# Performance work log

Hardware: AMD Instinct MI355X
Metric: run time of the kernel (lower is better)

Reference implementation:

```python
import jax, jax.numpy as jnp
import numpy as np

N_IMG = 512
N_ANGLES = 180


def _bilinear(img, sy, sx):
    """Bilinear sample img at float coords (sy, sx); zero outside the image."""
    n = img.shape[0]
    y0 = jnp.floor(sy)
    x0 = jnp.floor(sx)
    wy = sy - y0
    wx = sx - x0
    y0i = y0.astype(jnp.int32)
    x0i = x0.astype(jnp.int32)

    def gather(yi, xi):
        valid = (yi >= 0) & (yi < n) & (xi >= 0) & (xi < n)
        yc = jnp.clip(yi, 0, n - 1)
        xc = jnp.clip(xi, 0, n - 1)
        return jnp.where(valid, img[yc, xc], jnp.zeros((), img.dtype))

    v00 = gather(y0i, x0i)
    v01 = gather(y0i, x0i + 1)
    v10 = gather(y0i + 1, x0i)
    v11 = gather(y0i + 1, x0i + 1)
    return (v00 * (1 - wy) * (1 - wx) + v01 * (1 - wy) * wx
            + v10 * wy * (1 - wx) + v11 * wy * wx)


def _radon(img, angles):
    """skimage-style radon: rotate image by each angle, sum along axis 0.
    Returns sinogram of shape (n_detectors, n_angles) = (N, len(angles))."""
    n = img.shape[0]
    c = (n - 1) * 0.5  # rotation about image center
    coords = jnp.arange(n, dtype=img.dtype) - c
    yc, xc = jnp.meshgrid(coords, coords, indexing="ij")  # (N, N)

    def one_angle(theta_deg):
        t = jnp.deg2rad(theta_deg.astype(img.dtype))
        co, si = jnp.cos(t), jnp.sin(t)
        # inverse-rotation sampling coordinates (CCW rotation of the image)
        sx = co * xc + si * yc + c
        sy = -si * xc + co * yc + c
        rotated = _bilinear(img, sy, sx)  # (N, N)
        return rotated.sum(axis=0)        # projection along detector rows -> (N,)

    sino = jax.vmap(one_angle)(angles)  # (n_angles, N)
    return sino.T                        # (N, n_angles)


def setup_inputs() -> dict:
    key = jax.random.key(0)
    img = jax.random.uniform(key, (N_IMG, N_IMG), dtype=jnp.float32)  # nonnegative PET activity
    angles = jnp.arange(N_ANGLES, dtype=jnp.int32)  # degrees 0..179 (skimage default)
    return {"img": img, "angles": angles}


def reference(img, angles):
    return _radon(img, angles)
```

## Files before the change

kernel.cpp:

```cpp
#include <hip/hip_runtime.h>
#include <hip/hip_fp16.h>
#include <stdint.h>

#define N 512
#define NA 180
#define TD 64
#define TI 512
#define TW 96
#define TILE_DW (36 * 256)
#define PP 708
#define PR 704
#define POFF 96

#define WS_IMGPB  0
#define WS_IMGTPB (PR * PP)
#define WS_TAB    (2 * PR * PP)
#define WS_FLAGS  (WS_TAB + 4 * NA)

typedef _Float16 hh2 __attribute__((ext_vector_type(2)));
union H2U { uint32_t u; hh2 h; };

__device__ __forceinline__ hh2 cvt_pkrtz(float a, float b) {
    return __builtin_bit_cast(hh2, __builtin_amdgcn_cvt_pkrtz(a, b));
}

__device__ __forceinline__ void load16_to_lds(const uint32_t* g, uint32_t* l) {
    __builtin_amdgcn_global_load_lds(
        (const __attribute__((address_space(1))) void*)g,
        (__attribute__((address_space(3))) void*)l,
        16 , 0 , 0 );
}

__global__ __launch_bounds__(512) void pad_kernel(const float* __restrict__ img,
                                                  const int* __restrict__ angles,
                                                  uint32_t* __restrict__ imgPB,
                                                  uint32_t* __restrict__ imgTPB,
                                                  float4* __restrict__ tab,
                                                  int* __restrict__ flags) {
    __shared__ float lds[65 * 66];
    const int tid  = threadIdx.x;
    const int lane = tid & 63;
    const int wq   = tid >> 6;
    const int bx = blockIdx.x, by = blockIdx.y;
    const int b  = by * 11 + bx;

    if (b == 120 && tid < NA) {
        float t = (float)angles[tid] * 0.017453292519943295f;
        float si = sinf(t), co = cosf(t);
        int useT = fabsf(si) > fabsf(co);
        float4 e;
        if (useT) { e.x = co; e.y = -si; e.z = si; e.w = co; }
        else      { e.x = si; e.y = co;  e.z = co; e.w = -si; }
        tab[tid] = e;
        flags[tid] = useT;
    }

    for (int idx = tid; idx < 65 * 65; idx += 512) {
        int r = idx / 65, cc = idx - r * 65;
        int y = by * 64 + r - POFF, x = bx * 64 + cc - POFF;
        bool in = ((unsigned)y < N) && ((unsigned)x < N);
        lds[r * 66 + cc] = in ? img[y * N + x] : 0.0f;
    }
    __syncthreads();
#pragma unroll
    for (int j = 0; j < 8; ++j) {
        int r = wq * 8 + j;
        float v0 = lds[r * 66 + lane], v1 = lds[r * 66 + lane + 1];
        __half2 h = __halves2half2(__float2half(v0), __float2half(v1));
        imgPB[(size_t)(by * 64 + r) * PP + bx * 64 + lane] = *(uint32_t*)&h;
        float t0 = lds[lane * 66 + r], t1 = lds[(lane + 1) * 66 + r];
        __half2 ht = __halves2half2(__float2half(t0), __float2half(t1));
        imgTPB[(size_t)(bx * 64 + r) * PP + by * 64 + lane] = *(uint32_t*)&ht;
    }
}

__global__ __launch_bounds__(512, 8) void radon_kernel(const uint32_t* __restrict__ imgPB,
                                                       const uint32_t* __restrict__ imgTPB,
                                                       const float4* __restrict__ tab,
                                                       const int* __restrict__ flags,
                                                       float* __restrict__ out) {
    __shared__ uint32_t tile[TILE_DW];

    const int tid  = threadIdx.x;
    const int lane = tid & 63;
    const int wave = tid >> 6;
    const int d0 = blockIdx.x * TD;
    const int a  = blockIdx.y;
    const int rot = (blockIdx.x + blockIdx.y) & 7;

    const float c = 255.5f;
    const float4 tb = tab[a];
    const float au = tb.x, bus = tb.y, av = tb.z, bvs = tb.w;

    const float xc0 = (float)d0 - c, xc1 = (float)(d0 + TD - 1) - c;
    const float buA = fmaf(bus, xc0, c), buB = fmaf(bus, xc1, c);
    const float bvA = fmaf(bvs, xc0, c), bvB = fmaf(bvs, xc1, c);
    const float buMin = fminf(buA, buB), buMax = fmaxf(buA, buB);
    const float bvMin = fminf(bvA, bvB), bvMax = fmaxf(bvA, bvB);

    const uint32_t* __restrict__ src = flags[a] ? imgTPB : imgPB;

    const float xcl = (float)(d0 + lane) - c;
    const float buLb = fmaf(bus, xcl, c);
    const float bvLb = fmaf(bvs, xcl, c);

    const int t0g  = wave * 256 + (lane << 2);
    const int q0   = t0g / TW;
    const int c0   = t0g - q0 * TW;
    const int goff0 = q0 * PP + c0;

    float s = 0.0f;
    for (int p8 = 0; p8 < 8; ++p8) {
        const int ph = (p8 + rot) & 7;
        const int ip = ph * 64;
        const float fi0 = (float)ip - c, fi1 = (float)(ip + 63) - c;
        const float fiLoU = (au >= 0.0f) ? fi0 : fi1, fiHiU = (au >= 0.0f) ? fi1 : fi0;
        const float fiLoV = (av >= 0.0f) ? fi0 : fi1, fiHiV = (av >= 0.0f) ? fi1 : fi0;
        const float umin = fmaf(au, fiLoU, buMin), umax = fmaf(au, fiHiU, buMax);
        const float vmin = fmaf(av, fiLoV, bvMin), vmax = fmaf(av, fiHiV, bvMax);
        if (umin > (float)N || umax < -1.0f || vmin > (float)N || vmax < -1.0f)
            continue;

        const int ub0 = (((int)floorf(umin)) - 1) & ~3;
        const int vb  = ((int)floorf(vmin)) - 1;
        const int rows = ((int)floorf(vmax)) + 3 - vb;
        const int nch  = (rows * TW + 255) >> 8;

        __syncthreads();
        {
            const uint32_t* gb = src + (vb + POFF) * PP + (ub0 + POFF) + goff0;
            int cc = c0;
#pragma unroll
            for (int st = 0; st < 5; ++st) {
                int chunk = st * 8 + wave;
                if (chunk < nch) load16_to_lds(gb, &tile[chunk * 256]);
                cc += 32;
                int wrap = (cc >= TW);
                cc = wrap ? cc - TW : cc;
                gb += 21 * PP + 32 + (wrap ? (PP - TW) : 0);
            }
        }
        __syncthreads();
        {
            const float buL = buLb - (float)ub0;
            const float bvL = bvLb - (float)vb;
            const float fiw = (float)(ip + wave * 8) - c;
            float u = fmaf(au, fiw, buL);
            float v = fmaf(av, fiw, bvL);
#pragma unroll
            for (int k = 0; k < 8; ++k) {
                float wx = __builtin_amdgcn_fractf(u);
                float wy = __builtin_amdgcn_fractf(v);
                int iu = (int)u, iv = (int)v;
                int ai = iv * TW + iu;
                H2U P0, P1;
                P0.u = tile[ai];
                P1.u = tile[ai + TW];
                hh2 wy2 = cvt_pkrtz(wy, wy);
                hh2 m   = wy2 * (P1.h - P0.h) + P0.h;
                hh2 wv  = cvt_pkrtz(1.0f - wx, wx);
                s = __builtin_amdgcn_fdot2(wv, m, s, false);
                u += au;
                v += av;
            }
        }
    }

    __syncthreads();
    float* ft = (float*)tile;
    ft[tid] = s;
    __syncthreads();
    if (tid < 64) {
        float r = ft[tid]       + ft[tid + 64]  + ft[tid + 128] + ft[tid + 192]
                + ft[tid + 256] + ft[tid + 320] + ft[tid + 384] + ft[tid + 448];
        out[(d0 + tid) * NA + a] = r;
    }
}

extern "C" void kernel_launch(void* const* d_in, const int* in_sizes, int n_in,
                              void* d_out, int out_size, void* d_ws, size_t ws_size,
                              hipStream_t stream) {
    const float* img  = (const float*)d_in[0];
    const int* angles = (const int*)d_in[1];
    float* out = (float*)d_out;
    float* ws  = (float*)d_ws;

    uint32_t* imgPB  = (uint32_t*)(ws + WS_IMGPB);
    uint32_t* imgTPB = (uint32_t*)(ws + WS_IMGTPB);
    float4*   tab    = (float4*)(ws + WS_TAB);
    int*      flags  = (int*)(ws + WS_FLAGS);

    dim3 pgrid(11, 11);
    pad_kernel<<<pgrid, 512, 0, stream>>>(img, angles, imgPB, imgTPB, tab, flags);

    dim3 grid(N / TD, NA);
    radon_kernel<<<grid, 512, 0, stream>>>(imgPB, imgTPB, tab, flags, out);
}
```

Baseline: 90.40 us.

## Double-buffer LDS tiles in radon kernel and shrink pad kernel blocks

```diff
diff --git a/kernel.cpp b/kernel.cpp
--- a/kernel.cpp
+++ b/kernel.cpp
@@ -5,7 +5,6 @@
 #define N 512
 #define NA 180
 #define TD 64
-#define TI 512
 #define TW 96
 #define TILE_DW (36 * 256)
 #define PP 708
@@ -31,20 +30,17 @@
         16 , 0 , 0 );
 }
 
-__global__ __launch_bounds__(512) void pad_kernel(const float* __restrict__ img,
+__global__ __launch_bounds__(256) void pad_kernel(const float* __restrict__ img,
                                                   const int* __restrict__ angles,
                                                   uint32_t* __restrict__ imgPB,
                                                   uint32_t* __restrict__ imgTPB,
                                                   float4* __restrict__ tab,
                                                   int* __restrict__ flags) {
-    __shared__ float lds[65 * 66];
-    const int tid  = threadIdx.x;
-    const int lane = tid & 63;
-    const int wq   = tid >> 6;
+    __shared__ float lds[33 * 34];
+    const int tid = threadIdx.x;
     const int bx = blockIdx.x, by = blockIdx.y;
-    const int b  = by * 11 + bx;
-
-    if (b == 120 && tid < NA) {
+
+    if (bx == 0 && by == 0 && tid < NA) {
         float t = (float)angles[tid] * 0.017453292519943295f;
         float si = sinf(t), co = cosf(t);
         int useT = fabsf(si) > fabsf(co);
@@ -55,38 +51,38 @@
         flags[tid] = useT;
     }
 
-    for (int idx = tid; idx < 65 * 65; idx += 512) {
-        int r = idx / 65, cc = idx - r * 65;
-        int y = by * 64 + r - POFF, x = bx * 64 + cc - POFF;
+    for (int idx = tid; idx < 33 * 33; idx += 256) {
+        int r = idx / 33, cc = idx - r * 33;
+        int y = by * 32 + r - POFF, x = bx * 32 + cc - POFF;
         bool in = ((unsigned)y < N) && ((unsigned)x < N);
-        lds[r * 66 + cc] = in ? img[y * N + x] : 0.0f;
+        lds[r * 34 + cc] = in ? img[y * N + x] : 0.0f;
     }
     __syncthreads();
+    const int r0 = tid >> 5, cl = tid & 31;
 #pragma unroll
-    for (int j = 0; j < 8; ++j) {
-        int r = wq * 8 + j;
-        float v0 = lds[r * 66 + lane], v1 = lds[r * 66 + lane + 1];
+    for (int j = 0; j < 4; ++j) {
+        int row = j * 8 + r0;
+        float v0 = lds[row * 34 + cl], v1 = lds[row * 34 + cl + 1];
         __half2 h = __halves2half2(__float2half(v0), __float2half(v1));
-        imgPB[(size_t)(by * 64 + r) * PP + bx * 64 + lane] = *(uint32_t*)&h;
-        float t0 = lds[lane * 66 + r], t1 = lds[(lane + 1) * 66 + r];
+        imgPB[(size_t)(by * 32 + row) * PP + bx * 32 + cl] = *(uint32_t*)&h;
+        float t0 = lds[cl * 34 + row], t1 = lds[(cl + 1) * 34 + row];
         __half2 ht = __halves2half2(__float2half(t0), __float2half(t1));
-        imgTPB[(size_t)(bx * 64 + r) * PP + by * 64 + lane] = *(uint32_t*)&ht;
-    }
-}
-
-__global__ __launch_bounds__(512, 8) void radon_kernel(const uint32_t* __restrict__ imgPB,
+        imgTPB[(size_t)(bx * 32 + row) * PP + by * 32 + cl] = *(uint32_t*)&ht;
+    }
+}
+
+__global__ __launch_bounds__(512, 4) void radon_kernel(const uint32_t* __restrict__ imgPB,
                                                        const uint32_t* __restrict__ imgTPB,
                                                        const float4* __restrict__ tab,
                                                        const int* __restrict__ flags,
                                                        float* __restrict__ out) {
-    __shared__ uint32_t tile[TILE_DW];
+    __shared__ uint32_t tile[2 * TILE_DW];
 
     const int tid  = threadIdx.x;
     const int lane = tid & 63;
     const int wave = tid >> 6;
     const int d0 = blockIdx.x * TD;
     const int a  = blockIdx.y;
-    const int rot = (blockIdx.x + blockIdx.y) & 7;
 
     const float c = 255.5f;
     const float4 tb = tab[a];
@@ -109,44 +105,62 @@
     const int c0   = t0g - q0 * TW;
     const int goff0 = q0 * PP + c0;
 
-    float s = 0.0f;
-    for (int p8 = 0; p8 < 8; ++p8) {
-        const int ph = (p8 + rot) & 7;
-        const int ip = ph * 64;
+    auto params = [&](int p, int& ub0, int& vb, int& nch) -> bool {
+        const int ip = p * 64;
         const float fi0 = (float)ip - c, fi1 = (float)(ip + 63) - c;
         const float fiLoU = (au >= 0.0f) ? fi0 : fi1, fiHiU = (au >= 0.0f) ? fi1 : fi0;
         const float fiLoV = (av >= 0.0f) ? fi0 : fi1, fiHiV = (av >= 0.0f) ? fi1 : fi0;
         const float umin = fmaf(au, fiLoU, buMin), umax = fmaf(au, fiHiU, buMax);
         const float vmin = fmaf(av, fiLoV, bvMin), vmax = fmaf(av, fiHiV, bvMax);
         if (umin > (float)N || umax < -1.0f || vmin > (float)N || vmax < -1.0f)
-            continue;
-
-        const int ub0 = (((int)floorf(umin)) - 1) & ~3;
-        const int vb  = ((int)floorf(vmin)) - 1;
-        const int rows = ((int)floorf(vmax)) + 3 - vb;
-        const int nch  = (rows * TW + 255) >> 8;
-
+            return false;
+        ub0 = (((int)floorf(umin)) - 1) & ~3;
+        vb  = ((int)floorf(vmin)) - 1;
+        int rows = ((int)floorf(vmax)) + 3 - vb;
+        nch = (rows * TW + 255) >> 8;
+        return true;
+    };
+
+    auto stage = [&](int ub0, int vb, int nch, int base) {
+        const uint32_t* gb = src + (vb + POFF) * PP + (ub0 + POFF) + goff0;
+        int cc = c0;
+#pragma unroll
+        for (int st = 0; st < 5; ++st) {
+            int chunk = st * 8 + wave;
+            if (chunk < nch) load16_to_lds(gb, &tile[base + chunk * 256]);
+            cc += 32;
+            int wrap = (cc >= TW);
+            cc = wrap ? cc - TW : cc;
+            gb += 21 * PP + 32 + (wrap ? (PP - TW) : 0);
+        }
+    };
+
+    float s = 0.0f;
+
+    int pc = -1, ub0c = 0, vbc = 0, nchc = 0;
+    for (int p = 0; p < 8; ++p) {
+        if (params(p, ub0c, vbc, nchc)) { pc = p; break; }
+    }
+
+    int base = 0;
+    if (pc >= 0) {
+        stage(ub0c, vbc, nchc, base);
         __syncthreads();
+    }
+    while (pc >= 0) {
+        int pn = -1, ub0n = 0, vbn = 0, nchn = 0;
+        for (int p = pc + 1; p < 8; ++p) {
+            if (params(p, ub0n, vbn, nchn)) { pn = p; break; }
+        }
+        if (pn >= 0) stage(ub0n, vbn, nchn, base ^ TILE_DW);
+
         {
-            const uint32_t* gb = src + (vb + POFF) * PP + (ub0 + POFF) + goff0;
-            int cc = c0;
-#pragma unroll
-            for (int st = 0; st < 5; ++st) {
-                int chunk = st * 8 + wave;
-                if (chunk < nch) load16_to_lds(gb, &tile[chunk * 256]);
-                cc += 32;
-                int wrap = (cc >= TW);
-                cc = wrap ? cc - TW : cc;
-                gb += 21 * PP + 32 + (wrap ? (PP - TW) : 0);
-            }
-        }
-        __syncthreads();
-        {
-            const float buL = buLb - (float)ub0;
-            const float bvL = bvLb - (float)vb;
-            const float fiw = (float)(ip + wave * 8) - c;
+            const float buL = buLb - (float)ub0c;
+            const float bvL = bvLb - (float)vbc;
+            const float fiw = (float)(pc * 64 + wave * 8) - c;
             float u = fmaf(au, fiw, buL);
             float v = fmaf(av, fiw, bvL);
+            const uint32_t* tl = tile + base;
 #pragma unroll
             for (int k = 0; k < 8; ++k) {
                 float wx = __builtin_amdgcn_fractf(u);
@@ -154,8 +168,8 @@
                 int iu = (int)u, iv = (int)v;
                 int ai = iv * TW + iu;
                 H2U P0, P1;
-                P0.u = tile[ai];
-                P1.u = tile[ai + TW];
+                P0.u = tl[ai];
+                P1.u = tl[ai + TW];
                 hh2 wy2 = cvt_pkrtz(wy, wy);
                 hh2 m   = wy2 * (P1.h - P0.h) + P0.h;
                 hh2 wv  = cvt_pkrtz(1.0f - wx, wx);
@@ -164,6 +178,9 @@
                 v += av;
             }
         }
+        __syncthreads();
+        pc = pn; ub0c = ub0n; vbc = vbn; nchc = nchn;
+        base ^= TILE_DW;
     }
 
     __syncthreads();
@@ -190,8 +207,8 @@
     float4*   tab    = (float4*)(ws + WS_TAB);
     int*      flags  = (int*)(ws + WS_FLAGS);
 
-    dim3 pgrid(11, 11);
-    pad_kernel<<<pgrid, 512, 0, stream>>>(img, angles, imgPB, imgTPB, tab, flags);
+    dim3 pgrid(22, 22);
+    pad_kernel<<<pgrid, 256, 0, stream>>>(img, angles, imgPB, imgTPB, tab, flags);
 
     dim3 grid(N / TD, NA);
     radon_kernel<<<grid, 512, 0, stream>>>(imgPB, imgTPB, tab, flags, out);
```

Result: slower. 94.00 us (+4.0%).
